# Performance work log

Hardware: AMD Instinct MI355X
Metric: run time of the kernel (lower is better)

## Reference

```python
import jax, jax.numpy as jnp
import numpy as np

EMBED = 256
HEADS = 8
LEVELS = 4
POINTS = 4
HEAD_DIM = EMBED // HEADS
SHAPES = [(100, 100), (50, 50), (25, 25), (13, 13)]  # (H, W) per level
NUM_KEYS = sum(h * w for h, w in SHAPES)  # 13294
LEVEL_STARTS = np.cumsum([0] + [h * w for h, w in SHAPES])[:-1]
B, Q = 8, 900


def _offset_bias():
    # Faithful reproduction of the torch _reset_parameters sampling_offsets bias.
    th = np.arange(HEADS, dtype=np.float32) * (2.0 * np.pi / HEADS)
    g = np.stack([np.cos(th), np.sin(th)], -1)
    g = g / np.abs(g).max(-1, keepdims=True)
    g = np.tile(g[:, None, None, :], (1, LEVELS, POINTS, 1))
    g = g * np.arange(1, POINTS + 1, dtype=np.float32)[None, None, :, None]
    return jnp.asarray(g.reshape(-1), dtype=jnp.float32)


def setup_inputs() -> dict:
    key = jax.random.key(0)
    ks = jax.random.split(key, 12)
    s = 1.0 / np.sqrt(EMBED)
    return {
        "query": jax.random.normal(ks[0], (B, Q, EMBED), jnp.float32),
        "reference_points": jax.random.uniform(ks[1], (B, Q, LEVELS, 2), jnp.float32),
        "value": jax.random.normal(ks[2], (B, NUM_KEYS, EMBED), jnp.float32),
        "spatial_shapes": jnp.asarray(np.array(SHAPES, dtype=np.int32)),
        "level_start_index": jnp.asarray(LEVEL_STARTS.astype(np.int32)),
        "W_off": jax.random.normal(ks[3], (EMBED, HEADS * LEVELS * POINTS * 2), jnp.float32) * 0.01,
        "b_off": _offset_bias(),
        "W_attn": jax.random.normal(ks[4], (EMBED, HEADS * LEVELS * POINTS), jnp.float32) * 0.01,
        "b_attn": jnp.zeros((HEADS * LEVELS * POINTS,), jnp.float32),
        "W_val": jax.random.normal(ks[5], (EMBED, EMBED), jnp.float32) * s,
        "b_val": jnp.zeros((EMBED,), jnp.float32),
        "W_out": jax.random.normal(ks[6], (EMBED, EMBED), jnp.float32) * s,
        "b_out": jnp.zeros((EMBED,), jnp.float32),
    }


def _bilinear(vflat, x, y, H, W):
    # vflat: [BH, H*W, D]; x, y: [BH, Q, P] in unnormalized pixel coords.
    # grid_sample(mode='bilinear', padding_mode='zeros', align_corners=False)
    BH, Qn, Pn = x.shape
    D = vflat.shape[-1]
    x0f = jnp.floor(x); y0f = jnp.floor(y)
    wx = x - x0f; wy = y - y0f
    x0 = x0f.astype(jnp.int32); y0 = y0f.astype(jnp.int32)

    def gather(xi, yi):
        inb = (xi >= 0) & (xi < W) & (yi >= 0) & (yi < H)
        idx = jnp.clip(yi, 0, H - 1) * W + jnp.clip(xi, 0, W - 1)
        g = jnp.take_along_axis(vflat, idx.reshape(BH, Qn * Pn, 1), axis=1)
        return g.reshape(BH, Qn, Pn, D) * inb[..., None].astype(vflat.dtype)

    v00 = gather(x0, y0)
    v01 = gather(x0 + 1, y0)
    v10 = gather(x0, y0 + 1)
    v11 = gather(x0 + 1, y0 + 1)
    return (v00 * ((1 - wx) * (1 - wy))[..., None]
            + v01 * (wx * (1 - wy))[..., None]
            + v10 * ((1 - wx) * wy)[..., None]
            + v11 * (wx * wy)[..., None])


def _msda(value_hd, shapes_np, starts_np, loc, attw):
    # value_hd: [B, K, H, D]; loc: [B, Q, H, L, P, 2]; attw: [B, Q, H, L, P]
    Bn, K, Hn, D = value_hd.shape
    Qn, Pn = loc.shape[1], loc.shape[4]
    out = jnp.zeros((Bn * Hn, Qn, D), value_hd.dtype)
    for l, (Hl, Wl) in enumerate(shapes_np):
        s = int(starts_np[l])
        v = value_hd[:, s:s + Hl * Wl]                      # [B, Hl*Wl, H, D]
        v = v.reshape(Bn, Hl * Wl, Hn, D).transpose(0, 2, 1, 3)
        vflat = v.reshape(Bn * Hn, Hl * Wl, D)
        # sampling_grid = 2*loc - 1; grid_sample align_corners=False -> x = loc*W - 0.5
        lx = loc[:, :, :, l, :, 0].transpose(0, 2, 1, 3).reshape(Bn * Hn, Qn, Pn)
        ly = loc[:, :, :, l, :, 1].transpose(0, 2, 1, 3).reshape(Bn * Hn, Qn, Pn)
        samp = _bilinear(vflat, lx * Wl - 0.5, ly * Hl - 0.5, Hl, Wl)  # [BH,Q,P,D]
        w = attw[:, :, :, l, :].transpose(0, 2, 1, 3).reshape(Bn * Hn, Qn, Pn)
        out = out + jnp.einsum('bqpd,bqp->bqd', samp, w)
    return out.reshape(Bn, Hn, Qn, D).transpose(0, 2, 1, 3).reshape(Bn, Qn, Hn * D)


def reference(query, reference_points, value, spatial_shapes, level_start_index,
              W_off, b_off, W_attn, b_attn, W_val, b_val, W_out, b_out):
    shapes_np = np.asarray(spatial_shapes)
    starts_np = np.asarray(level_start_index)
    Bn, Qn, _ = query.shape
    K = value.shape[1]

    v = value @ W_val + b_val                              # [B, K, E]
    v = v.reshape(Bn, K, HEADS, HEAD_DIM)

    off = (query @ W_off + b_off).reshape(Bn, Qn, HEADS, LEVELS, POINTS, 2)
    aw = (query @ W_attn + b_attn).reshape(Bn, Qn, HEADS, LEVELS * POINTS)
    aw = jax.nn.softmax(aw, axis=-1).reshape(Bn, Qn, HEADS, LEVELS, POINTS)

    # offset_normalizer = (W, H) per level
    norm = jnp.asarray(shapes_np[:, ::-1].astype(np.float32)).reshape(1, 1, 1, LEVELS, 1, 2)
    loc = reference_points[:, :, None, :, None, :] + off / norm  # [B,Q,H,L,P,2]

    out = _msda(v, shapes_np, starts_np, loc, aw)          # [B, Q, E]
    return out @ W_out + b_out
```

## Files before the change

### kernel.cpp

```cpp
#include <hip/hip_runtime.h>
#include <hip/hip_bf16.h>
#include <math.h>
#include <type_traits>

#define BATCH 8
#define QLEN 900
#define HEADS 8
#define LEVELS 4
#define POINTS 4
#define NUM_KEYS 13294
#define BQ (BATCH * QLEN)
#define MROWS_V (BATCH * NUM_KEYS)
#define VTILES (MROWS_V / 16)
#define VBLOCKS 512
#define TPB 13

__constant__ const int c_LH[4] = {100, 50, 25, 13};
__constant__ const int c_LW[4] = {100, 50, 25, 13};
__constant__ const int c_LS[4] = {0, 10000, 12500, 13125};

typedef __attribute__((ext_vector_type(8))) short bfrag;
typedef __attribute__((ext_vector_type(4))) float ffrag;

static __device__ __forceinline__ unsigned short f2bf(float f) {
    __hip_bfloat16 h = __float2bfloat16(f);
    return *(unsigned short*)&h;
}
static __device__ __forceinline__ float bf2f(unsigned int u16) {
    unsigned int v = u16 << 16;
    float f;
    __builtin_memcpy(&f, &v, 4);
    return f;
}
static __device__ __forceinline__ unsigned long long pack4bf(float4 v) {
    return (unsigned long long)f2bf(v.x)
         | ((unsigned long long)f2bf(v.y) << 16)
         | ((unsigned long long)f2bf(v.z) << 32)
         | ((unsigned long long)f2bf(v.w) << 48);
}

__global__ __launch_bounds__(256)
void prep_kernel(const float* __restrict__ W_val, const float* __restrict__ W_off,
                 const float* __restrict__ W_attn, const float* __restrict__ W_out,
                 const float* __restrict__ b_off, const float* __restrict__ b_attn,
                 unsigned short* __restrict__ Wv, unsigned short* __restrict__ Woa,
                 unsigned short* __restrict__ Wo, float* __restrict__ boa) {
    const int id = blockIdx.x * 256 + threadIdx.x;
    if (id < 65536) {
        const int n = id >> 8, k = id & 255;
        Wv[id] = f2bf(W_val[k * 256 + n]);
    } else if (id < 131072) {
        const int t = id - 65536;
        const int n = t >> 8, k = t & 255;
        Woa[t] = f2bf(W_off[k * 256 + n]);
    } else if (id < 163840) {
        const int t = id - 131072;
        const int n = t >> 8, k = t & 255;
        Woa[65536 + t] = f2bf(W_attn[k * 128 + n]);
    } else if (id < 229376) {
        const int t = id - 163840;
        const int n = t >> 8, k = t & 255;
        Wo[t] = f2bf(W_out[k * 256 + n]);
    } else if (id < 229760) {
        const int t = id - 229376;
        boa[t] = (t < 256) ? b_off[t] : b_attn[t - 256];
    }
}

#define VSTEP(T, LREG)                                                        \
  do {                                                                        \
    const char* abuf = (const char*)&Abuf[0][0] + rb * 8192;                  \
    ffrag acc[4];                                                             \
    _Pragma("unroll")                                                         \
    for (int j_ = 0; j_ < 4; ++j_) acc[j_] = (ffrag){0.f, 0.f, 0.f, 0.f};     \
    _Pragma("unroll")                                                         \
    for (int ks_ = 0; ks_ < 8; ++ks_) {                                       \
      const int ub_ = (ks_ * 64 + quad * 16) ^ ((ln & 7) << 4);               \
      const bfrag af_ = *(const bfrag*)(abuf + ln * 512 + ub_);               \
      _Pragma("unroll")                                                       \
      for (int j_ = 0; j_ < 4; ++j_)                                          \
        acc[j_] = __builtin_amdgcn_mfma_f32_16x16x32_bf16(af_, b[j_][ks_],    \
                                                          acc[j_], 0, 0, 0); \
    }                                                                         \
    if ((T) + 1 < t1) {                                                       \
      const int wb_ = (rb + 1 == 3) ? 0 : rb + 1;                             \
      char* dbuf_ = (char*)&Abuf[0][0] + wb_ * 8192;                          \
      _Pragma("unroll")                                                       \
      for (int i_ = 0; i_ < 4; ++i_)                                          \
        *(unsigned long long*)(dbuf_ + dsoff[i_]) = pack4bf(LREG[i_]);        \
      if ((T) + 3 < t1) {                                                     \
        const float4* ap_ = Af4 + (size_t)((T) + 3) * 1024 + tid;             \
        _Pragma("unroll")                                                     \
        for (int i_ = 0; i_ < 4; ++i_) LREG[i_] = ap_[i_ * 256];              \
      }                                                                       \
    }                                                                         \
    const int rowb_ = (T) * 16 + quad * 4;                                    \
    _Pragma("unroll")                                                         \
    for (int j_ = 0; j_ < 4; ++j_) {                                          \
      const int col_ = n0 + j_ * 16 + ln;                                     \
      _Pragma("unroll")                                                       \
      for (int r_ = 0; r_ < 4; ++r_)                                          \
        C[(size_t)(rowb_ + r_) * 256 + col_] = f2bf(acc[j_][r_] + bj[j_]);    \
    }                                                                         \
    asm volatile("s_waitcnt lgkmcnt(0)" ::: "memory");                        \
    __builtin_amdgcn_s_barrier();                                             \
    rb = (rb + 1 == 3) ? 0 : rb + 1;                                          \
  } while (0)

__global__ __launch_bounds__(256, 2)
void gemm_val_stream(const float* __restrict__ A, const unsigned short* __restrict__ WT,
                     const float* __restrict__ bias, unsigned short* __restrict__ C) {
    __shared__ __align__(16) unsigned short Abuf[3][16 * 256];
    const int tid = threadIdx.x;
    const int wave = tid >> 6;
    const int lane = tid & 63;
    const int ln = lane & 15;
    const int quad = lane >> 4;
    const int n0 = wave * 64;

    bfrag b[4][8];
#pragma unroll
    for (int j = 0; j < 4; ++j) {
        const unsigned short* bp = WT + (size_t)(n0 + j * 16 + ln) * 256 + quad * 8;
#pragma unroll
        for (int ks = 0; ks < 8; ++ks) b[j][ks] = *(const bfrag*)(bp + ks * 32);
    }
    float bj[4];
#pragma unroll
    for (int j = 0; j < 4; ++j) bj[j] = bias[n0 + j * 16 + ln];

    const int t0 = blockIdx.x * TPB;
    const int t1 = min(t0 + TPB, VTILES);
    if (t0 >= t1) return;

    int dsoff[4];
#pragma unroll
    for (int i = 0; i < 4; ++i) {
        const int f = i * 256 + tid;
        const int r = f >> 6;
        const int cb = (f & 63) * 8;
        dsoff[i] = r * 512 + (cb ^ ((r & 7) << 4));
    }

    const float4* Af4 = (const float4*)A;

    float4 L0[4], L1[4];
    {
        const float4* ap = Af4 + (size_t)t0 * 1024 + tid;
        float4 P[4];
#pragma unroll
        for (int i = 0; i < 4; ++i) P[i] = ap[i * 256];
#pragma unroll
        for (int i = 0; i < 4; ++i)
            *(unsigned long long*)((char*)&Abuf[0][0] + dsoff[i]) = pack4bf(P[i]);
    }
    if (t0 + 1 < t1) {
        const float4* ap = Af4 + (size_t)(t0 + 1) * 1024 + tid;
#pragma unroll
        for (int i = 0; i < 4; ++i) L0[i] = ap[i * 256];
    }
    if (t0 + 2 < t1) {
        const float4* ap = Af4 + (size_t)(t0 + 2) * 1024 + tid;
#pragma unroll
        for (int i = 0; i < 4; ++i) L1[i] = ap[i * 256];
    }
    asm volatile("s_waitcnt lgkmcnt(0)" ::: "memory");
    __builtin_amdgcn_s_barrier();

    int rb = 0;
    int t = t0;
    while (t + 1 < t1) {
        VSTEP(t, L0);
        VSTEP(t + 1, L1);
        t += 2;
    }
    if (t < t1) VSTEP(t, L0);
}

#define GST 72

template <typename AT, typename CT>
__global__ __launch_bounds__(256)
void gemm_mfma(const AT* __restrict__ A, const unsigned short* __restrict__ WT,
               const float* __restrict__ bias, CT* __restrict__ C,
               int M, int ldc) {
    __shared__ unsigned short As[64 * GST];
    __shared__ unsigned short Bs[128 * GST];
    const int tid = threadIdx.x;
    const int wave = tid >> 6;
    const int lane = tid & 63;
    const int ln = lane & 15;
    const int quad = lane >> 4;
    const int m0 = blockIdx.x * 64;
    const int n0 = blockIdx.y * 128;

    ffrag acc[8];
#pragma unroll
    for (int j = 0; j < 8; ++j) acc[j] = (ffrag){0.f, 0.f, 0.f, 0.f};

    const int ar = tid >> 2;
    const int akc = (tid & 3) * 16;
    const int brow = tid >> 1;
    const int bkc = (tid & 1) * 32;
    const bool a_ok = (m0 + ar) < M;
    const AT* a_src = A + (size_t)(m0 + ar) * 256 + akc;
    const unsigned short* b_src = WT + (size_t)(n0 + brow) * 256 + bkc;

    for (int k0 = 0; k0 < 256; k0 += 64) {
        unsigned short* adst = &As[ar * GST + akc];
        if constexpr (std::is_same<AT, float>::value) {
            float4 f0, f1, f2, f3;
            if (a_ok) {
                const float4* p = (const float4*)(a_src + k0);
                f0 = p[0]; f1 = p[1]; f2 = p[2]; f3 = p[3];
            } else {
                f0 = make_float4(0.f, 0.f, 0.f, 0.f);
                f1 = f0; f2 = f0; f3 = f0;
            }
            float v[16] = {f0.x, f0.y, f0.z, f0.w, f1.x, f1.y, f1.z, f1.w,
                           f2.x, f2.y, f2.z, f2.w, f3.x, f3.y, f3.z, f3.w};
            unsigned short u[16];
#pragma unroll
            for (int i = 0; i < 16; ++i) u[i] = f2bf(v[i]);
            ((uint4*)adst)[0] = ((uint4*)u)[0];
            ((uint4*)adst)[1] = ((uint4*)u)[1];
        } else {
            uint4 u0, u1;
            if (a_ok) {
                const uint4* p = (const uint4*)(a_src + k0);
                u0 = p[0]; u1 = p[1];
            } else {
                u0 = make_uint4(0, 0, 0, 0);
                u1 = u0;
            }
            ((uint4*)adst)[0] = u0;
            ((uint4*)adst)[1] = u1;
        }
        {
            const uint4* src = (const uint4*)(b_src + k0);
            uint4* dst = (uint4*)&Bs[brow * GST + bkc];
#pragma unroll
            for (int i = 0; i < 4; ++i) dst[i] = src[i];
        }
        __syncthreads();

#pragma unroll
        for (int ks = 0; ks < 2; ++ks) {
            const int koff = ks * 32 + quad * 8;
            bfrag af = *(const bfrag*)&As[(wave * 16 + ln) * GST + koff];
#pragma unroll
            for (int j = 0; j < 8; ++j) {
                bfrag bf = *(const bfrag*)&Bs[(j * 16 + ln) * GST + koff];
                acc[j] = __builtin_amdgcn_mfma_f32_16x16x32_bf16(af, bf, acc[j], 0, 0, 0);
            }
        }
        __syncthreads();
    }

#pragma unroll
    for (int j = 0; j < 8; ++j) {
        const int col = n0 + j * 16 + ln;
        const float bb = bias[col];
#pragma unroll
        for (int r = 0; r < 4; ++r) {
            const int row = m0 + wave * 16 + quad * 4 + r;
            if (row < M) {
                const float v = acc[j][r] + bb;
                if constexpr (std::is_same<CT, unsigned short>::value) {
                    C[(size_t)row * ldc + col] = f2bf(v);
                } else {
                    C[(size_t)row * ldc + col] = v;
                }
            }
        }
    }
}

__global__ __launch_bounds__(256, 4)
void msda_sample_kernel(const float* __restrict__ offattn,
                        const float* __restrict__ rp,
                        const unsigned short* __restrict__ vb,
                        unsigned short* __restrict__ outb) {
    const int bq0 = blockIdx.x * 8;
    const int tid = threadIdx.x;

    __shared__ float s_w[8][128];
    __shared__ float s_x[8][128];
    __shared__ float s_y[8][128];

#pragma unroll
    for (int i = 0; i < 4; ++i) {
        const int e = i * 256 + tid;
        const int q = e >> 7, t = e & 127;
        s_w[q][t] = offattn[(size_t)(bq0 + q) * 384 + 256 + t];
    }
    __syncthreads();

    if (tid < 64) {
        const int q = tid >> 3, h = tid & 7;
        float m = -1e30f;
#pragma unroll
        for (int i = 0; i < 16; ++i) m = fmaxf(m, s_w[q][h * 16 + i]);
        float e[16];
        float s = 0.f;
#pragma unroll
        for (int i = 0; i < 16; ++i) {
            e[i] = expf(s_w[q][h * 16 + i] - m);
            s += e[i];
        }
        const float inv = 1.f / s;
#pragma unroll
        for (int i = 0; i < 16; ++i) s_w[q][h * 16 + i] = e[i] * inv;
    }

#pragma unroll
    for (int i = 0; i < 4; ++i) {
        const int e = i * 256 + tid;
        const int q = e >> 7, t = e & 127;
        const int h = t >> 4, l = (t >> 2) & 3, p = t & 3;
        const int bq = bq0 + q;
        const float2 off = *(const float2*)(offattn + (size_t)bq * 384 + h * 32 + l * 8 + p * 2);
        const float Wl = (float)c_LW[l];
        const float Hl = (float)c_LH[l];
        const float rx = rp[((size_t)bq * 4 + l) * 2 + 0];
        const float ry = rp[((size_t)bq * 4 + l) * 2 + 1];
        s_x[q][t] = (rx + off.x / Wl) * Wl - 0.5f;
        s_y[q][t] = (ry + off.y / Hl) * Hl - 0.5f;
    }
    __syncthreads();

    const int q = tid >> 5;
    const int s = tid & 31;
    const int h = s >> 2;
    const int dp = s & 3;
    const int bq = bq0 + q;
    const int b = bq / QLEN;
    const unsigned short* vbase = vb + (size_t)b * NUM_KEYS * 256 + h * 32 + dp * 8;

    float acc[8];
#pragma unroll
    for (int d = 0; d < 8; ++d) acc[d] = 0.f;

#pragma unroll
    for (int l = 0; l < LEVELS; ++l) {
        const int Hl = c_LH[l];
        const int Wl = c_LW[l];
        const int s0 = c_LS[l];
#pragma unroll 2
        for (int p = 0; p < POINTS; ++p) {
            const int t2 = h * 16 + l * 4 + p;
            const float x = s_x[q][t2];
            const float y = s_y[q][t2];
            const float w = s_w[q][t2];
            const float x0f = floorf(x);
            const float y0f = floorf(y);
            const float wx = x - x0f;
            const float wy = y - y0f;
            const int x0 = (int)x0f;
            const int y0 = (int)y0f;
            const float mx0 = ((unsigned)x0 < (unsigned)Wl) ? 1.f : 0.f;
            const float mx1 = ((unsigned)(x0 + 1) < (unsigned)Wl) ? 1.f : 0.f;
            const float my0 = ((unsigned)y0 < (unsigned)Hl) ? 1.f : 0.f;
            const float my1 = ((unsigned)(y0 + 1) < (unsigned)Hl) ? 1.f : 0.f;
            const int xc0 = min(max(x0, 0), Wl - 1);
            const int xc1 = min(max(x0 + 1, 0), Wl - 1);
            const int yc0 = min(max(y0, 0), Hl - 1);
            const int yc1 = min(max(y0 + 1, 0), Hl - 1);
            const float a00 = w * (1.f - wx) * (1.f - wy) * mx0 * my0;
            const float a01 = w * wx * (1.f - wy) * mx1 * my0;
            const float a10 = w * (1.f - wx) * wy * mx0 * my1;
            const float a11 = w * wx * wy * mx1 * my1;
            const size_t k00 = (size_t)(s0 + yc0 * Wl + xc0) * 256;
            const size_t k01 = (size_t)(s0 + yc0 * Wl + xc1) * 256;
            const size_t k10 = (size_t)(s0 + yc1 * Wl + xc0) * 256;
            const size_t k11 = (size_t)(s0 + yc1 * Wl + xc1) * 256;
            const uint4 r00 = *(const uint4*)(vbase + k00);
            const uint4 r01 = *(const uint4*)(vbase + k01);
            const uint4 r10 = *(const uint4*)(vbase + k10);
            const uint4 r11 = *(const uint4*)(vbase + k11);
            const unsigned int w00[4] = {r00.x, r00.y, r00.z, r00.w};
            const unsigned int w01[4] = {r01.x, r01.y, r01.z, r01.w};
            const unsigned int w10[4] = {r10.x, r10.y, r10.z, r10.w};
            const unsigned int w11[4] = {r11.x, r11.y, r11.z, r11.w};
#pragma unroll
            for (int i = 0; i < 4; ++i) {
                const float v00l = bf2f(w00[i] & 0xffffu), v00h = bf2f(w00[i] >> 16);
                const float v01l = bf2f(w01[i] & 0xffffu), v01h = bf2f(w01[i] >> 16);
                const float v10l = bf2f(w10[i] & 0xffffu), v10h = bf2f(w10[i] >> 16);
                const float v11l = bf2f(w11[i] & 0xffffu), v11h = bf2f(w11[i] >> 16);
                acc[i * 2 + 0] = fmaf(a00, v00l, fmaf(a01, v01l, fmaf(a10, v10l, fmaf(a11, v11l, acc[i * 2 + 0]))));
                acc[i * 2 + 1] = fmaf(a00, v00h, fmaf(a01, v01h, fmaf(a10, v10h, fmaf(a11, v11h, acc[i * 2 + 1]))));
            }
        }
    }

    unsigned short o[8];
#pragma unroll
    for (int d = 0; d < 8; ++d) o[d] = f2bf(acc[d]);
    *(uint4*)(outb + (size_t)bq * 256 + h * 32 + dp * 8) = *(uint4*)o;
}

extern "C" void kernel_launch(void* const* d_in, const int* in_sizes, int n_in,
                              void* d_out, int out_size, void* d_ws, size_t ws_size,
                              hipStream_t stream) {
    const float* query  = (const float*)d_in[0];
    const float* rp     = (const float*)d_in[1];
    const float* value  = (const float*)d_in[2];
    const float* W_off  = (const float*)d_in[5];
    const float* b_off  = (const float*)d_in[6];
    const float* W_attn = (const float*)d_in[7];
    const float* b_attn = (const float*)d_in[8];
    const float* W_val  = (const float*)d_in[9];
    const float* b_val  = (const float*)d_in[10];
    const float* W_out  = (const float*)d_in[11];
    const float* b_out  = (const float*)d_in[12];
    float* out = (float*)d_out;

    char* w = (char*)d_ws;
    unsigned short* ws_vb = (unsigned short*)w;
    w += (size_t)MROWS_V * 256 * 2;
    float* ws_offattn = (float*)w;
    w += (size_t)BQ * 384 * 4;
    unsigned short* ws_msda = (unsigned short*)w;
    w += (size_t)BQ * 256 * 2;
    unsigned short* ws_Wv = (unsigned short*)w;  w += 256 * 256 * 2;
    unsigned short* ws_Woa = (unsigned short*)w; w += 384 * 256 * 2;
    unsigned short* ws_Wo = (unsigned short*)w;  w += 256 * 256 * 2;
    float* ws_boa = (float*)w;

    prep_kernel<<<898, 256, 0, stream>>>(W_val, W_off, W_attn, W_out,
                                         b_off, b_attn, ws_Wv, ws_Woa, ws_Wo, ws_boa);

    gemm_val_stream<<<VBLOCKS, 256, 0, stream>>>(value, ws_Wv, b_val, ws_vb);

    {
        dim3 grid((BQ + 63) / 64, 3);
        gemm_mfma<float, float><<<grid, 256, 0, stream>>>(
            query, ws_Woa, ws_boa, ws_offattn, BQ, 384);
    }
    msda_sample_kernel<<<BQ / 8, 256, 0, stream>>>(ws_offattn, rp, ws_vb, ws_msda);

    {
        dim3 grid((BQ + 63) / 64, 2);
        gemm_mfma<unsigned short, float><<<grid, 256, 0, stream>>>(
            ws_msda, ws_Wo, b_out, out, BQ, 256);
    }
}
```

Before: 255.7 us.

## Store projected values head-major and batch all point gathers per level

The value-projection GEMM now writes its output in a [batch, head, key, 32] layout instead of [batch, key, 256]. Each head's samples then fall in a compact 64-byte-per-key region, which should improve cache locality for the bilinear gathers. The sampling kernel also computes all four points' weights and indices first, then issues all 16 gathers before accumulating, to raise memory-level parallelism. Launch bounds drop from 4 to 3 blocks per SM to make room for the extra registers, trading occupancy for more loads in flight, and the GEMM epilogue stores become more scattered.

```diff
diff --git a/kernel.cpp b/kernel.cpp
--- a/kernel.cpp
+++ b/kernel.cpp
@@ -96,11 +96,17 @@
     }                                                                         \
     const int rowb_ = (T) * 16 + quad * 4;                                    \
     _Pragma("unroll")                                                         \
-    for (int j_ = 0; j_ < 4; ++j_) {                                          \
-      const int col_ = n0 + j_ * 16 + ln;                                     \
+    for (int r_ = 0; r_ < 4; ++r_) {                                          \
+      const unsigned row_ = rowb_ + r_;                                       \
+      const unsigned bb_ = row_ / NUM_KEYS;                                   \
+      const unsigned key_ = row_ - bb_ * NUM_KEYS;                            \
       _Pragma("unroll")                                                       \
-      for (int r_ = 0; r_ < 4; ++r_)                                          \
-        C[(size_t)(rowb_ + r_) * 256 + col_] = f2bf(acc[j_][r_] + bj[j_]);    \
+      for (int j_ = 0; j_ < 4; ++j_) {                                        \
+        const int col_ = n0 + j_ * 16 + ln;                                   \
+        const int h_ = col_ >> 5, d_ = col_ & 31;                             \
+        C[((size_t)(bb_ * 8 + h_) * NUM_KEYS + key_) * 32 + d_] =             \
+            f2bf(acc[j_][r_] + bj[j_]);                                       \
+      }                                                                       \
     }                                                                         \
     asm volatile("s_waitcnt lgkmcnt(0)" ::: "memory");                        \
     __builtin_amdgcn_s_barrier();                                             \
@@ -276,7 +282,7 @@
     }
 }
 
-__global__ __launch_bounds__(256, 4)
+__global__ __launch_bounds__(256, 3)
 void msda_sample_kernel(const float* __restrict__ offattn,
                         const float* __restrict__ rp,
                         const unsigned short* __restrict__ vb,
@@ -335,7 +341,7 @@
     const int dp = s & 3;
     const int bq = bq0 + q;
     const int b = bq / QLEN;
-    const unsigned short* vbase = vb + (size_t)b * NUM_KEYS * 256 + h * 32 + dp * 8;
+    const unsigned short* vbase = vb + (size_t)(b * 8 + h) * NUM_KEYS * 32 + dp * 8;
 
     float acc[8];
 #pragma unroll
@@ -346,8 +352,11 @@
         const int Hl = c_LH[l];
         const int Wl = c_LW[l];
         const int s0 = c_LS[l];
-#pragma unroll 2
-        for (int p = 0; p < POINTS; ++p) {
+
+        float aw[4][4];
+        int   kk[4][4];
+#pragma unroll
+        for (int p = 0; p < 4; ++p) {
             const int t2 = h * 16 + l * 4 + p;
             const float x = s_x[q][t2];
             const float y = s_y[q][t2];
@@ -366,28 +375,37 @@
             const int xc1 = min(max(x0 + 1, 0), Wl - 1);
             const int yc0 = min(max(y0, 0), Hl - 1);
             const int yc1 = min(max(y0 + 1, 0), Hl - 1);
-            const float a00 = w * (1.f - wx) * (1.f - wy) * mx0 * my0;
-            const float a01 = w * wx * (1.f - wy) * mx1 * my0;
-            const float a10 = w * (1.f - wx) * wy * mx0 * my1;
-            const float a11 = w * wx * wy * mx1 * my1;
-            const size_t k00 = (size_t)(s0 + yc0 * Wl + xc0) * 256;
-            const size_t k01 = (size_t)(s0 + yc0 * Wl + xc1) * 256;
-            const size_t k10 = (size_t)(s0 + yc1 * Wl + xc0) * 256;
-            const size_t k11 = (size_t)(s0 + yc1 * Wl + xc1) * 256;
-            const uint4 r00 = *(const uint4*)(vbase + k00);
-            const uint4 r01 = *(const uint4*)(vbase + k01);
-            const uint4 r10 = *(const uint4*)(vbase + k10);
-            const uint4 r11 = *(const uint4*)(vbase + k11);
-            const unsigned int w00[4] = {r00.x, r00.y, r00.z, r00.w};
-            const unsigned int w01[4] = {r01.x, r01.y, r01.z, r01.w};
-            const unsigned int w10[4] = {r10.x, r10.y, r10.z, r10.w};
-            const unsigned int w11[4] = {r11.x, r11.y, r11.z, r11.w};
+            aw[p][0] = w * (1.f - wx) * (1.f - wy) * mx0 * my0;
+            aw[p][1] = w * wx * (1.f - wy) * mx1 * my0;
+            aw[p][2] = w * (1.f - wx) * wy * mx0 * my1;
+            aw[p][3] = w * wx * wy * mx1 * my1;
+            kk[p][0] = s0 + yc0 * Wl + xc0;
+            kk[p][1] = s0 + yc0 * Wl + xc1;
+            kk[p][2] = s0 + yc1 * Wl + xc0;
+            kk[p][3] = s0 + yc1 * Wl + xc1;
+        }
+
+        uint4 R[4][4];
+#pragma unroll
+        for (int p = 0; p < 4; ++p) {
+#pragma unroll
+            for (int c = 0; c < 4; ++c)
+                R[p][c] = *(const uint4*)(vbase + (size_t)kk[p][c] * 32);
+        }
+
+#pragma unroll
+        for (int p = 0; p < 4; ++p) {
+            const unsigned int w0[4] = {R[p][0].x, R[p][0].y, R[p][0].z, R[p][0].w};
+            const unsigned int w1[4] = {R[p][1].x, R[p][1].y, R[p][1].z, R[p][1].w};
+            const unsigned int w2[4] = {R[p][2].x, R[p][2].y, R[p][2].z, R[p][2].w};
+            const unsigned int w3[4] = {R[p][3].x, R[p][3].y, R[p][3].z, R[p][3].w};
+            const float a00 = aw[p][0], a01 = aw[p][1], a10 = aw[p][2], a11 = aw[p][3];
 #pragma unroll
             for (int i = 0; i < 4; ++i) {
-                const float v00l = bf2f(w00[i] & 0xffffu), v00h = bf2f(w00[i] >> 16);
-                const float v01l = bf2f(w01[i] & 0xffffu), v01h = bf2f(w01[i] >> 16);
-                const float v10l = bf2f(w10[i] & 0xffffu), v10h = bf2f(w10[i] >> 16);
-                const float v11l = bf2f(w11[i] & 0xffffu), v11h = bf2f(w11[i] >> 16);
+                const float v00l = bf2f(w0[i] & 0xffffu), v00h = bf2f(w0[i] >> 16);
+                const float v01l = bf2f(w1[i] & 0xffffu), v01h = bf2f(w1[i] >> 16);
+                const float v10l = bf2f(w2[i] & 0xffffu), v10h = bf2f(w2[i] >> 16);
+                const float v11l = bf2f(w3[i] & 0xffffu), v11h = bf2f(w3[i] >> 16);
                 acc[i * 2 + 0] = fmaf(a00, v00l, fmaf(a01, v01l, fmaf(a10, v10l, fmaf(a11, v11l, acc[i * 2 + 0]))));
                 acc[i * 2 + 1] = fmaf(a00, v00h, fmaf(a01, v01h, fmaf(a10, v10h, fmaf(a11, v11h, acc[i * 2 + 1]))));
             }
```

Result: slower. 507.1 us (+98.3%).
